# Kernel optimization log

Hardware: AMD Instinct MI355X
Metric: run time of the kernel (lower is better)

Reference implementation:

```python
import jax, jax.numpy as jnp
import numpy as np

B, N = 4, 512
H, NH, L = 64, 4, 3
HD = H // NH          # 16
NODE_F, EDGE_F = 18, 7
H4 = H // 4           # 16
FF = 4 * H            # 256


def _ln(x, g, b, eps=1e-5):
    m = jnp.mean(x, axis=-1, keepdims=True)
    v = jnp.mean((x - m) ** 2, axis=-1, keepdims=True)
    return (x - m) * jax.lax.rsqrt(v + eps) * g + b


def _leaky(x):
    return jnp.where(x >= 0, x, 0.2 * x)


def _spd(edge_mask):
    # Vectorized Floyd-Warshall, mirrors GraphTransformer._compute_spd_matrix
    n = edge_mask.shape[1]
    spd = jnp.where(edge_mask, 1.0, float(n)).astype(jnp.float32)
    i = jnp.arange(n)
    spd = spd.at[:, i, i].set(0.0)
    def body(k, s):
        col = jax.lax.dynamic_slice_in_dim(s, k, 1, axis=2)  # [B,N,1]
        row = jax.lax.dynamic_slice_in_dim(s, k, 1, axis=1)  # [B,1,N]
        return jnp.minimum(s, col + row)
    return jax.lax.fori_loop(0, n, body, spd)


def setup_inputs() -> dict:
    key = jax.random.key(0)
    ks = iter(jax.random.split(key, 64))
    def nrm(shape, s):
        return jax.random.normal(next(ks), shape, jnp.float32) * s
    inp = {}
    inp["node_features"] = jax.random.normal(next(ks), (B, N, NODE_F), jnp.float32)
    inp["edge_features"] = jax.random.normal(next(ks), (B, N, N, EDGE_F), jnp.float32)
    nm = jax.random.uniform(next(ks), (B, N)) < 0.9
    inp["node_mask"] = nm.at[:, 0].set(True)
    inp["edge_mask"] = jax.random.uniform(next(ks), (B, N, N)) < 0.05
    s_h = 1.0 / np.sqrt(H)
    inp["node_proj_w"] = nrm((NODE_F, H), 0.2)
    inp["node_proj_b"] = jnp.zeros((H,), jnp.float32)
    inp["edge_proj_w"] = nrm((EDGE_F, H), 0.2)
    inp["edge_proj_b"] = jnp.zeros((H,), jnp.float32)
    inp["wq"] = nrm((L, H, H), s_h)
    inp["wk"] = nrm((L, H, H), s_h)
    inp["wv"] = nrm((L, H, H), s_h)
    inp["eb1_w"] = nrm((L, H, H4), s_h)
    inp["eb1_b"] = jnp.zeros((L, H4), jnp.float32)
    inp["eb_ln_g"] = jnp.ones((L, H4), jnp.float32)
    inp["eb_ln_b"] = jnp.zeros((L, H4), jnp.float32)
    inp["eb2_w"] = nrm((L, H4, NH), 0.2)
    inp["eb2_b"] = jnp.zeros((L, NH), jnp.float32)
    inp["spd1_w"] = nrm((L, 1, H4), 0.5)
    inp["spd1_b"] = jnp.zeros((L, H4), jnp.float32)
    inp["spd2_w"] = nrm((L, H4, NH), 0.2)
    inp["spd2_b"] = jnp.zeros((L, NH), jnp.float32)
    inp["wo_w"] = nrm((L, H, H), s_h)
    inp["wo_b"] = jnp.zeros((L, H), jnp.float32)
    inp["ln1_g"] = jnp.ones((L, H), jnp.float32)
    inp["ln1_b"] = jnp.zeros((L, H), jnp.float32)
    inp["ln2_g"] = jnp.ones((L, H), jnp.float32)
    inp["ln2_b"] = jnp.zeros((L, H), jnp.float32)
    inp["ffn1_w"] = nrm((L, H, FF), s_h)
    inp["ffn1_b"] = jnp.zeros((L, FF), jnp.float32)
    inp["ffn2_w"] = nrm((L, FF, H), 1.0 / np.sqrt(FF))
    inp["ffn2_b"] = jnp.zeros((L, H), jnp.float32)
    inp["score1_w"] = nrm((2 * H, H), 1.0 / np.sqrt(2 * H))
    inp["score1_b"] = jnp.zeros((H,), jnp.float32)
    inp["score_ln_g"] = jnp.ones((H,), jnp.float32)
    inp["score_ln_b"] = jnp.zeros((H,), jnp.float32)
    inp["score2_w"] = nrm((H, 1), 0.1)
    inp["score2_b"] = jnp.zeros((1,), jnp.float32)
    return inp


def reference(node_features, edge_features, node_mask, edge_mask,
              node_proj_w, node_proj_b, edge_proj_w, edge_proj_b,
              wq, wk, wv,
              eb1_w, eb1_b, eb_ln_g, eb_ln_b, eb2_w, eb2_b,
              spd1_w, spd1_b, spd2_w, spd2_b,
              wo_w, wo_b, ln1_g, ln1_b, ln2_g, ln2_b,
              ffn1_w, ffn1_b, ffn2_w, ffn2_b,
              score1_w, score1_b, score_ln_g, score_ln_b, score2_w, score2_b):
    NEG = -1000000000.0
    h = node_features @ node_proj_w + node_proj_b            # [B,N,H]
    e = edge_features @ edge_proj_w + edge_proj_b            # [B,N,N,H]
    spd = _spd(edge_mask)
    spd_n = (jnp.clip(spd, 0.0, 10.0) / 10.0)[..., None]      # [B,N,N,1]
    scale = 1.0 / np.sqrt(HD)
    for l in range(L):
        Q = (h @ wq[l]).reshape(B, N, NH, HD)
        K = (h @ wk[l]).reshape(B, N, NH, HD)
        V = (h @ wv[l]).reshape(B, N, NH, HD)
        scores = jnp.einsum('bihd,bjhd->bhij', Q, K) * scale  # [B,NH,N,N]
        x = _leaky(_ln(e @ eb1_w[l] + eb1_b[l], eb_ln_g[l], eb_ln_b[l]))
        edge_bias = jnp.transpose(x @ eb2_w[l] + eb2_b[l], (0, 3, 1, 2))
        sb = _leaky(spd_n @ spd1_w[l] + spd1_b[l]) @ spd2_w[l] + spd2_b[l]
        spd_bias = jnp.transpose(sb, (0, 3, 1, 2))
        bias = jnp.where(edge_mask[:, None, :, :], edge_bias, spd_bias)
        scores = jnp.where(node_mask[:, None, None, :], scores + bias, NEG)
        attn = jax.nn.softmax(scores, axis=-1)
        out = jnp.einsum('bhij,bjhd->bihd', attn, V).reshape(B, N, H)
        out = out @ wo_w[l] + wo_b[l]
        h = _ln(h + out, ln1_g[l], ln1_b[l])
        ff = jax.nn.gelu(h @ ffn1_w[l] + ffn1_b[l], approximate=False) @ ffn2_w[l] + ffn2_b[l]
        h = _ln(h + ff, ln2_g[l], ln2_b[l])
    h_ego = jnp.broadcast_to(h[:, :1, :], (B, N - 1, H))
    hc = jnp.concatenate([h_ego, h[:, 1:, :]], axis=-1)       # [B,N-1,2H]
    x = _leaky(_ln(hc @ score1_w + score1_b, score_ln_g, score_ln_b))
    logits = (x @ score2_w + score2_b)[..., 0]                # [B,N-1]
    cand_mask = node_mask[:, 1:]
    no_cand = ~jnp.any(cand_mask, axis=-1)
    cand_mask = cand_mask.at[:, 0].set(cand_mask[:, 0] | no_cand)
    logits = jnp.where(cand_mask, logits, NEG)
    probs = jax.nn.softmax(logits, axis=-1)
    return probs, h
```

## Files before the change

kernel.cpp:

```cpp
#include <hip/hip_runtime.h>
#include <math.h>

typedef unsigned long long u64;
typedef unsigned int u32;

__device__ __forceinline__ float wsum(float x) {
#pragma unroll
    for (int o = 1; o < 64; o <<= 1) x += __shfl_xor(x, o);
    return x;
}
__device__ __forceinline__ float wmaxr(float x) {
#pragma unroll
    for (int o = 1; o < 64; o <<= 1) x = fmaxf(x, __shfl_xor(x, o));
    return x;
}

__global__ __launch_bounds__(256) void kA(
    const int* __restrict__ em, const float* __restrict__ nf,
    const float* __restrict__ npw, const float* __restrict__ npb,
    u64* __restrict__ adj, u32* __restrict__ elist, u32* __restrict__ rowCnt,
    float* __restrict__ hbuf)
{
    int t = threadIdx.x, wv = t >> 6, lane = t & 63;
    int g = blockIdx.x * 4 + wv;
    const int* emr = em + (size_t)g * 512;
    u32 run = 0;
#pragma unroll
    for (int s = 0; s < 8; ++s) {
        int j = s * 64 + lane;
        int v = emr[j];
        u64 bal = __ballot(v != 0);
        if (v != 0) {
            u32 slot = run + (u32)__popcll(bal & ((1ULL << lane) - 1ULL));
            if (slot < 96u) elist[g * 96 + slot] = (u32)j;
        }
        if (lane == 0) adj[(size_t)g * 8 + s] = bal;
        run += (u32)__popcll(bal);
    }
    if (lane == 0) rowCnt[g] = run < 96u ? run : 96u;
    float acc = npb[lane];
    const float* r = nf + (size_t)g * 18;
#pragma unroll
    for (int c = 0; c < 18; ++c) acc += r[c] * npw[c * 64 + lane];
    hbuf[(size_t)g * 64 + lane] = acc;
}

__global__ __launch_bounds__(256) void kB(
    const u64* __restrict__ adj, const float* __restrict__ ef,
    const u32* __restrict__ elist, const u32* __restrict__ rowCnt,
    const float* __restrict__ hbuf,
    const float* __restrict__ epw, const float* __restrict__ epb,
    const float* __restrict__ eb1w, const float* __restrict__ eb1b,
    const float* __restrict__ eblng, const float* __restrict__ eblnb,
    const float* __restrict__ eb2w, const float* __restrict__ eb2b,
    const float* __restrict__ wq, const float* __restrict__ wk, const float* __restrict__ wvw,
    unsigned char* __restrict__ spd, float* __restrict__ vals,
    float* __restrict__ Qb, float* __restrict__ KT, float* __restrict__ VT)
{
    __shared__ u64 adjL[4096 + 4 * 88];
    int t = threadIdx.x, wv = t >> 6, lane = t & 63;
    int g = blockIdx.x * 4 + wv;
    int b = g >> 9, srow = g & 511;
    {
        const float4* s = (const float4*)(adj + (size_t)b * 4096);
        float4* d = (float4*)adjL;
#pragma unroll
        for (int u = 0; u < 8; ++u) d[t + u * 256] = s[t + u * 256];
    }
    __syncthreads();
    u64* wb = adjL + 4096 + wv * 88;
    u64* vis = wb; u64* fro = wb + 8; u64* nxt = wb + 16; u64* dist8 = wb + 24;
    unsigned char* dist = (unsigned char*)dist8;
    dist8[lane] = 0x0A0A0A0A0A0A0A0AULL;
    if (lane < 8) { vis[lane] = 0ULL; fro[lane] = 0ULL; nxt[lane] = 0ULL; }
    __syncthreads();
    if (lane == 0) {
        dist[srow] = 0;
        vis[srow >> 6] = 1ULL << (srow & 63);
        fro[srow >> 6] = 1ULL << (srow & 63);
    }
    __syncthreads();
    for (int d = 1; d <= 9; ++d) {
        int c = lane >> 3, w = lane & 7;
        u64 f = fro[c];
        u64 acc = 0ULL;
        while (f) {
            int k = (c << 6) + __builtin_ctzll(f);
            f &= f - 1;
            acc |= adjL[k * 8 + w];
        }
        if (acc) atomicOr(&nxt[w], acc);
        __syncthreads();
        if (lane < 8) {
            u64 nw = nxt[lane] & ~vis[lane];
            vis[lane] |= nw; fro[lane] = nw; nxt[lane] = 0ULL;
            while (nw) {
                int j = (lane << 6) + __builtin_ctzll(nw);
                nw &= nw - 1;
                dist[j] = (unsigned char)d;
            }
        }
        __syncthreads();
    }
    ((u64*)(spd + (size_t)g * 512))[lane] = dist8[lane];
    {
        float hv = hbuf[(size_t)g * 64 + lane];
        float aq = 0.f, ak = 0.f, av = 0.f;
        for (int k = 0; k < 64; ++k) {
            float hk = __shfl(hv, k);
            aq += hk * wq[k * 64 + lane];
            ak += hk * wk[k * 64 + lane];
            av += hk * wvw[k * 64 + lane];
        }
        Qb[(size_t)g * 64 + lane] = aq;
        KT[((size_t)(b * 64 + lane)) * 512 + srow] = ak;
        VT[((size_t)(b * 64 + lane)) * 512 + srow] = av;
    }
    {
        u32 cnt = rowCnt[g];
        for (u32 s = lane; s < cnt; s += 64u) {
            u32 j = elist[g * 96 + s];
            const float* e7 = ef + ((size_t)g * 512 + j) * 7;
            float f0 = e7[0], f1 = e7[1], f2 = e7[2], f3 = e7[3], f4 = e7[4], f5 = e7[5], f6 = e7[6];
            float tt[3][16];
#pragma unroll
            for (int l = 0; l < 3; ++l)
#pragma unroll
                for (int c = 0; c < 16; ++c) tt[l][c] = eb1b[l * 16 + c];
            for (int k = 0; k < 64; ++k) {
                float ek = epb[k] + f0 * epw[k] + f1 * epw[64 + k] + f2 * epw[128 + k]
                         + f3 * epw[192 + k] + f4 * epw[256 + k] + f5 * epw[320 + k]
                         + f6 * epw[384 + k];
#pragma unroll
                for (int l = 0; l < 3; ++l) {
                    const float* W1 = eb1w + l * 1024 + k * 16;
#pragma unroll
                    for (int c = 0; c < 16; ++c) tt[l][c] += ek * W1[c];
                }
            }
#pragma unroll
            for (int l = 0; l < 3; ++l) {
                float m = 0.f;
#pragma unroll
                for (int c = 0; c < 16; ++c) m += tt[l][c];
                m *= 0.0625f;
                float var = 0.f;
#pragma unroll
                for (int c = 0; c < 16; ++c) { float d = tt[l][c] - m; var += d * d; }
                var *= 0.0625f;
                float inv = rsqrtf(var + 1e-5f);
#pragma unroll
                for (int c = 0; c < 16; ++c) {
                    float x = (tt[l][c] - m) * inv * eblng[l * 16 + c] + eblnb[l * 16 + c];
                    tt[l][c] = x >= 0.f ? x : 0.2f * x;
                }
#pragma unroll
                for (int hh = 0; hh < 4; ++hh) {
                    float a = eb2b[l * 4 + hh];
#pragma unroll
                    for (int c = 0; c < 16; ++c) a += tt[l][c] * eb2w[(l * 16 + c) * 4 + hh];
                    vals[(u32)(l * 4 + hh) * 196608u + (u32)g * 96u + s] = a;
                }
            }
        }
    }
}

__global__ __launch_bounds__(256, 2) void kL(
    const float* __restrict__ Qb, const float* __restrict__ KTin, const float* __restrict__ VTin,
    const unsigned char* __restrict__ spd, const u32* __restrict__ elist,
    const u32* __restrict__ rowCnt, const float* __restrict__ vals,
    const float* __restrict__ s1w, const float* __restrict__ s1b,
    const float* __restrict__ s2w, const float* __restrict__ s2b,
    const int* __restrict__ nm,
    const float* __restrict__ wow, const float* __restrict__ wob,
    const float* __restrict__ ln1g, const float* __restrict__ ln1b,
    const float* __restrict__ f1w, const float* __restrict__ f1b,
    const float* __restrict__ f2w, const float* __restrict__ f2b,
    const float* __restrict__ ln2g, const float* __restrict__ ln2b,
    const float* __restrict__ wqn, const float* __restrict__ wkn, const float* __restrict__ wvn,
    float* __restrict__ hbuf, float* __restrict__ QbOut,
    float* __restrict__ KTout, float* __restrict__ VTout,
    int l, float* __restrict__ out)
{
    __shared__ float kt[8192];
    __shared__ float bv[2048];
    __shared__ float ATTO[256];
    __shared__ unsigned char SPDl[2048];
    int t = threadIdx.x, wv = t >> 6, lane = t & 63;
    int blk = blockIdx.x;
    int g = blk * 4 + wv;
    int b = blk >> 7, srow = g & 511;
    float hv = hbuf[(size_t)g * 64 + lane];
    float qrow = Qb[(size_t)g * 64 + lane];
    {
        const u32* sp = (const u32*)(spd + (size_t)(blk * 4) * 512);
        u32* dd = (u32*)SPDl;
        dd[t] = sp[t]; dd[t + 256] = sp[t + 256];
    }
    float madd[8];
#pragma unroll
    for (int c = 0; c < 8; ++c) madd[c] = (nm[b * 512 + c * 64 + lane] != 0) ? 0.f : -1e9f;
    u32 cnt = rowCnt[g];
    u32 ej0 = 0, ej1 = 0;
    if (lane < (int)cnt) ej0 = elist[g * 96 + lane];
    if (lane + 64 < (int)cnt) ej1 = elist[g * 96 + lane + 64];

#pragma unroll 1
    for (int hh = 0; hh < 4; ++hh) {
        __syncthreads();
        {
            const float4* s = (const float4*)(KTin + ((size_t)(b * 64 + hh * 16)) * 512);
            float4* d = (float4*)kt;
#pragma unroll
            for (int u = 0; u < 8; ++u) d[t + u * 256] = s[t + u * 256];
        }
        float tval;
        {
            int li = lane < 11 ? lane : 10;
            float x = (float)li * 0.1f;
            float a = s2b[l * 4 + hh];
#pragma unroll
            for (int c = 0; c < 16; ++c) {
                float v = x * s1w[l * 16 + c] + s1b[l * 16 + c];
                v = v >= 0.f ? v : 0.2f * v;
                a += v * s2w[(l * 16 + c) * 4 + hh];
            }
            tval = a;
        }
#pragma unroll
        for (int p = 0; p < 2; ++p) {
            int i32 = t + p * 256;
            u32 w4 = ((const u32*)SPDl)[i32];
            float4 bb;
            bb.x = __shfl(tval, (int)(w4 & 255u));
            bb.y = __shfl(tval, (int)((w4 >> 8) & 255u));
            bb.z = __shfl(tval, (int)((w4 >> 16) & 255u));
            bb.w = __shfl(tval, (int)(w4 >> 24));
            ((float4*)bv)[i32] = bb;
        }
        __syncthreads();
        u32 vp = (u32)(l * 4 + hh) * 196608u;
        if (lane < (int)cnt) bv[wv * 512 + (int)(ej0 & 511u)] = vals[vp + (u32)g * 96u + lane];
        if (lane + 64 < (int)cnt) bv[wv * 512 + (int)(ej1 & 511u)] = vals[vp + (u32)g * 96u + lane + 64];
        float q[16];
#pragma unroll
        for (int d = 0; d < 16; ++d) q[d] = __shfl(qrow, hh * 16 + d);
        float sc[8];
        float mx = -3e38f;
#pragma unroll
        for (int c = 0; c < 8; ++c) {
            int j = c * 64 + lane;
            float s = 0.f;
#pragma unroll
            for (int d = 0; d < 16; ++d) s += q[d] * kt[d * 512 + j];
            s = s * 0.25f + bv[wv * 512 + j] + madd[c];
            sc[c] = s;
            mx = fmaxf(mx, s);
        }
        mx = wmaxr(mx);
        float sm = 0.f;
#pragma unroll
        for (int c = 0; c < 8; ++c) { sc[c] = __expf(sc[c] - mx); sm += sc[c]; }
        float sminv = 1.0f / wsum(sm);
#pragma unroll
        for (int c = 0; c < 8; ++c) sc[c] *= sminv;
        __syncthreads();
        {
            const float4* s = (const float4*)(VTin + ((size_t)(b * 64 + hh * 16)) * 512);
            float4* d = (float4*)kt;
#pragma unroll
            for (int u = 0; u < 8; ++u) d[t + u * 256] = s[t + u * 256];
        }
        __syncthreads();
        float acc[16];
#pragma unroll
        for (int d = 0; d < 16; ++d) acc[d] = 0.f;
#pragma unroll
        for (int c = 0; c < 8; ++c) {
            int j = c * 64 + lane;
#pragma unroll
            for (int d = 0; d < 16; ++d) acc[d] += sc[c] * kt[d * 512 + j];
        }
#pragma unroll
        for (int d = 0; d < 16; ++d) {
            acc[d] += __shfl_xor(acc[d], 16);
            acc[d] += __shfl_xor(acc[d], 32);
        }
        float* scr = bv + wv * 272;
        if (lane < 16) {
#pragma unroll
            for (int d = 0; d < 16; ++d) scr[lane * 17 + d] = acc[d];
        }
        if (lane < 16) {
            float o = 0.f;
#pragma unroll
            for (int m = 0; m < 16; ++m) o += scr[m * 17 + lane];
            ATTO[wv * 64 + hh * 16 + lane] = o;
        }
    }
    float h1;
    {
        float a = wob[l * 64 + lane];
        const float* Wo = wow + l * 4096;
        for (int k = 0; k < 64; ++k) a += ATTO[wv * 64 + k] * Wo[k * 64 + lane];
        float xx = a + hv;
        float mn = wsum(xx) * 0.015625f;
        float d = xx - mn;
        float var = wsum(d * d) * 0.015625f;
        h1 = d * rsqrtf(var + 1e-5f) * ln1g[l * 64 + lane] + ln1b[l * 64 + lane];
    }
    float hn;
    {
        const float* W1 = f1w + l * 16384;
        const float* W2 = f2w + l * 16384;
        float a1[4];
#pragma unroll
        for (int m = 0; m < 4; ++m) a1[m] = f1b[l * 256 + m * 64 + lane];
        for (int k = 0; k < 64; ++k) {
            float hk = __shfl(h1, k);
#pragma unroll
            for (int m = 0; m < 4; ++m) a1[m] += hk * W1[k * 256 + m * 64 + lane];
        }
        float ffv[4];
#pragma unroll
        for (int m = 0; m < 4; ++m) {
            float u = a1[m];
            ffv[m] = 0.5f * u * (1.0f + erff(u * 0.70710678118654752f));
        }
        float a2 = 0.f;
#pragma unroll 1
        for (int m = 0; m < 4; ++m) {
            for (int ll = 0; ll < 64; ++ll) {
                a2 += __shfl(ffv[m], ll) * W2[(m * 64 + ll) * 64 + lane];
            }
        }
        float xx = a2 + f2b[l * 64 + lane] + h1;
        float mn = wsum(xx) * 0.015625f;
        float d = xx - mn;
        float var = wsum(d * d) * 0.015625f;
        hn = d * rsqrtf(var + 1e-5f) * ln2g[l * 64 + lane] + ln2b[l * 64 + lane];
    }
    hbuf[(size_t)g * 64 + lane] = hn;
    if (l == 2) {
        out[2044 + (size_t)g * 64 + lane] = hn;
    } else {
        float aq = 0.f, ak = 0.f, av = 0.f;
        for (int k = 0; k < 64; ++k) {
            float hk = __shfl(hn, k);
            aq += hk * wqn[k * 64 + lane];
            ak += hk * wkn[k * 64 + lane];
            av += hk * wvn[k * 64 + lane];
        }
        QbOut[(size_t)g * 64 + lane] = aq;
        KTout[((size_t)(b * 64 + lane)) * 512 + srow] = ak;
        VTout[((size_t)(b * 64 + lane)) * 512 + srow] = av;
    }
}

__global__ __launch_bounds__(256) void kS(
    const float* __restrict__ hbuf,
    const float* __restrict__ s1w, const float* __restrict__ s1b,
    const float* __restrict__ lng, const float* __restrict__ lnb,
    const float* __restrict__ s2w, const float* __restrict__ s2b,
    float* __restrict__ logits)
{
    int t = threadIdx.x, wv = t >> 6, lane = t & 63;
    int wid = blockIdx.x * 4 + wv;
    if (wid >= 2044) return;
    int bb = wid / 511; int jj = wid % 511; int j = jj + 1;
    float ego = hbuf[(size_t)bb * 32768 + lane];
    float cand = hbuf[((size_t)(bb * 512 + j)) * 64 + lane];
    float acc = s1b[lane];
    for (int k = 0; k < 64; ++k) acc += __shfl(ego, k) * s1w[k * 64 + lane];
    for (int k = 0; k < 64; ++k) acc += __shfl(cand, k) * s1w[(64 + k) * 64 + lane];
    float mn = wsum(acc) * 0.015625f;
    float d = acc - mn;
    float var = wsum(d * d) * 0.015625f;
    float x = d * rsqrtf(var + 1e-5f) * lng[lane] + lnb[lane];
    x = x >= 0.f ? x : 0.2f * x;
    float p = wsum(x * s2w[lane]);
    if (lane == 0) logits[wid] = p + s2b[0];
}

__global__ __launch_bounds__(512) void kP(
    const float* __restrict__ logits, const int* __restrict__ nmask, float* __restrict__ out)
{
    __shared__ float red[512];
    __shared__ int anyf;
    int b = blockIdx.x; int t = threadIdx.x;
    bool cand = false;
    if (t < 511) cand = nmask[b * 512 + 1 + t] != 0;
    if (t == 0) anyf = 0;
    __syncthreads();
    if (cand) atomicOr(&anyf, 1);
    __syncthreads();
    if (t == 0 && anyf == 0) cand = true;
    float val = -3e38f;
    if (t < 511) val = cand ? logits[b * 511 + t] : -1e9f;
    red[t] = val; __syncthreads();
    for (int s = 256; s > 0; s >>= 1) { if (t < s) red[t] = fmaxf(red[t], red[t + s]); __syncthreads(); }
    float m = red[0]; __syncthreads();
    float p = (t < 511) ? __expf(val - m) : 0.f;
    red[t] = p; __syncthreads();
    for (int s = 256; s > 0; s >>= 1) { if (t < s) red[t] += red[t + s]; __syncthreads(); }
    float inv = 1.0f / red[0];
    if (t < 511) out[b * 511 + t] = p * inv;
}

extern "C" void kernel_launch(void* const* d_in, const int* in_sizes, int n_in,
                              void* d_out, int out_size, void* d_ws, size_t ws_size,
                              hipStream_t stream) {
    const float* nf    = (const float*)d_in[0];
    const float* ef    = (const float*)d_in[1];
    const int*   nm    = (const int*)d_in[2];
    const int*   em    = (const int*)d_in[3];
    const float* npw   = (const float*)d_in[4];
    const float* npb   = (const float*)d_in[5];
    const float* epw   = (const float*)d_in[6];
    const float* epb   = (const float*)d_in[7];
    const float* wq    = (const float*)d_in[8];
    const float* wk    = (const float*)d_in[9];
    const float* wv    = (const float*)d_in[10];
    const float* eb1w  = (const float*)d_in[11];
    const float* eb1b  = (const float*)d_in[12];
    const float* eblng = (const float*)d_in[13];
    const float* eblnb = (const float*)d_in[14];
    const float* eb2w  = (const float*)d_in[15];
    const float* eb2b  = (const float*)d_in[16];
    const float* s1wv  = (const float*)d_in[17];
    const float* s1bv  = (const float*)d_in[18];
    const float* s2wv  = (const float*)d_in[19];
    const float* s2bv  = (const float*)d_in[20];
    const float* wow   = (const float*)d_in[21];
    const float* wob   = (const float*)d_in[22];
    const float* ln1g  = (const float*)d_in[23];
    const float* ln1b  = (const float*)d_in[24];
    const float* ln2g  = (const float*)d_in[25];
    const float* ln2b  = (const float*)d_in[26];
    const float* f1w   = (const float*)d_in[27];
    const float* f1b   = (const float*)d_in[28];
    const float* f2w   = (const float*)d_in[29];
    const float* f2b   = (const float*)d_in[30];
    const float* sc1w  = (const float*)d_in[31];
    const float* sc1b  = (const float*)d_in[32];
    const float* sclng = (const float*)d_in[33];
    const float* sclnb = (const float*)d_in[34];
    const float* sc2w  = (const float*)d_in[35];
    const float* sc2b  = (const float*)d_in[36];

    char* W = (char*)d_ws;
    u64*   adj    = (u64*)(W + 0);
    unsigned char* spd = (unsigned char*)(W + 131072);
    u32*   elist  = (u32*)(W + 1179648);
    u32*   rowCnt = (u32*)(W + 1966080);
    float* vals   = (float*)(W + 1974272);
    float* hbuf   = (float*)(W + 11411456);
    float* Qb     = (float*)(W + 11935744);
    float* KT0    = (float*)(W + 12460032);
    float* VT0    = (float*)(W + 12984320);
    float* KT1    = (float*)(W + 13508608);
    float* VT1    = (float*)(W + 14032896);
    float* logits = (float*)(W + 14557184);

    float* out = (float*)d_out;

    kA<<<512, 256, 0, stream>>>(em, nf, npw, npb, adj, elist, rowCnt, hbuf);
    kB<<<512, 256, 0, stream>>>(adj, ef, elist, rowCnt, hbuf, epw, epb,
                                eb1w, eb1b, eblng, eblnb, eb2w, eb2b,
                                wq, wk, wv, spd, vals, Qb, KT0, VT0);
    kL<<<512, 256, 0, stream>>>(Qb, KT0, VT0, spd, elist, rowCnt, vals,
                                s1wv, s1bv, s2wv, s2bv, nm,
                                wow, wob, ln1g, ln1b, f1w, f1b, f2w, f2b, ln2g, ln2b,
                                wq + 4096, wk + 4096, wv + 4096,
                                hbuf, Qb, KT1, VT1, 0, out);
    kL<<<512, 256, 0, stream>>>(Qb, KT1, VT1, spd, elist, rowCnt, vals,
                                s1wv, s1bv, s2wv, s2bv, nm,
                                wow, wob, ln1g, ln1b, f1w, f1b, f2w, f2b, ln2g, ln2b,
                                wq + 8192, wk + 8192, wv + 8192,
                                hbuf, Qb, KT0, VT0, 1, out);
    kL<<<512, 256, 0, stream>>>(Qb, KT0, VT0, spd, elist, rowCnt, vals,
                                s1wv, s1bv, s2wv, s2bv, nm,
                                wow, wob, ln1g, ln1b, f1w, f1b, f2w, f2b, ln2g, ln2b,
                                wq, wk, wv,
                                hbuf, Qb, KT1, VT1, 2, out);
    kS<<<512, 256, 0, stream>>>(hbuf, sc1w, sc1b, sclng, sclnb, sc2w, sc2b, logits);
    kP<<<4, 512, 0, stream>>>(logits, nm, out);
}
```

Baseline: 336.8 us.

## Split attention per head, fold edge-bias weights, early-exit BFS, precompute ego projection

The per-layer kernel is split into a head-parallel attention kernel (2048 blocks) and a separate output/FFN kernel, which raises parallelism at the cost of an extra launch and an attention-output round trip through global memory. The edge-bias MLP folds the edge projection into the first bias layer via a precomputed 7x16 matrix held in shared memory. Edge work is pooled across the four warps of a block to balance load. The BFS exits early once all frontiers are empty and keeps distances in registers. The ego half of the scoring MLP is computed once per batch in the last layer instead of per candidate.

```diff
diff --git a/kernel.cpp b/kernel.cpp
--- a/kernel.cpp
+++ b/kernel.cpp
@@ -57,7 +57,13 @@
     unsigned char* __restrict__ spd, float* __restrict__ vals,
     float* __restrict__ Qb, float* __restrict__ KT, float* __restrict__ VT)
 {
-    __shared__ u64 adjL[4096 + 4 * 88];
+    __shared__ u64 adjL[4096];
+    __shared__ u64 bfsS[4][24];
+    __shared__ float MS[684];
+    __shared__ u32 pool[384];
+    __shared__ u32 offs[5];
+    __shared__ u32 cA[4];
+    __shared__ int votes[4];
     int t = threadIdx.x, wv = t >> 6, lane = t & 63;
     int g = blockIdx.x * 4 + wv;
     int b = g >> 9, srow = g & 511;
@@ -67,19 +73,31 @@
 #pragma unroll
         for (int u = 0; u < 8; ++u) d[t + u * 256] = s[t + u * 256];
     }
-    __syncthreads();
-    u64* wb = adjL + 4096 + wv * 88;
-    u64* vis = wb; u64* fro = wb + 8; u64* nxt = wb + 16; u64* dist8 = wb + 24;
-    unsigned char* dist = (unsigned char*)dist8;
-    dist8[lane] = 0x0A0A0A0A0A0A0A0AULL;
-    if (lane < 8) { vis[lane] = 0ULL; fro[lane] = 0ULL; nxt[lane] = 0ULL; }
-    __syncthreads();
-    if (lane == 0) {
-        dist[srow] = 0;
-        vis[srow >> 6] = 1ULL << (srow & 63);
-        fro[srow >> 6] = 1ULL << (srow & 63);
-    }
-    __syncthreads();
+    for (int u = t; u < 384; u += 256) {
+        int l = u >> 7, r = u & 127, f = r >> 4, c = r & 15;
+        const float* W1 = eb1w + l * 1024 + c;
+        float s;
+        if (f < 7) {
+            s = 0.f;
+            const float* ew = epw + f * 64;
+            for (int k = 0; k < 64; ++k) s += ew[k] * W1[k * 16];
+        } else {
+            s = eb1b[l * 16 + c];
+            for (int k = 0; k < 64; ++k) s += epb[k] * W1[k * 16];
+        }
+        MS[u] = s;
+    }
+    if (t < 192) MS[384 + t] = eb2w[t];
+    if (t < 48) { MS[576 + t] = eblng[t]; MS[624 + t] = eblnb[t]; }
+    if (t < 12) MS[672 + t] = eb2b[t];
+    u64* vis = &bfsS[wv][0]; u64* fro = vis + 8; u64* nxt = vis + 16;
+    if (lane < 8) {
+        u64 iv = (lane == (srow >> 6)) ? (1ULL << (srow & 63)) : 0ULL;
+        vis[lane] = iv; fro[lane] = iv; nxt[lane] = 0ULL;
+    }
+    __syncthreads();
+    u64 myDist = 0x0A0A0A0A0A0A0A0AULL;
+    if (lane == (srow >> 3)) myDist &= ~(0xFFULL << ((srow & 7) * 8));
     for (int d = 1; d <= 9; ++d) {
         int c = lane >> 3, w = lane & 7;
         u64 f = fro[c];
@@ -91,18 +109,25 @@
         }
         if (acc) atomicOr(&nxt[w], acc);
         __syncthreads();
+        u64 nw = 0ULL;
         if (lane < 8) {
-            u64 nw = nxt[lane] & ~vis[lane];
+            nw = nxt[lane] & ~vis[lane];
             vis[lane] |= nw; fro[lane] = nw; nxt[lane] = 0ULL;
-            while (nw) {
-                int j = (lane << 6) + __builtin_ctzll(nw);
-                nw &= nw - 1;
-                dist[j] = (unsigned char)d;
-            }
-        }
+        }
+        u64 bal = __ballot(nw != 0ULL);
+        if (lane == 0) votes[wv] = (bal != 0ULL) ? 1 : 0;
         __syncthreads();
-    }
-    ((u64*)(spd + (size_t)g * 512))[lane] = dist8[lane];
+        u64 fw = fro[lane >> 3];
+        u32 bits = (u32)(fw >> ((lane & 7) * 8)) & 0xFFu;
+        if (bits) {
+            u64 bm = 0ULL;
+#pragma unroll
+            for (int kk = 0; kk < 8; ++kk) if (bits & (1u << kk)) bm |= 0xFFULL << (8 * kk);
+            myDist = (myDist & ~bm) | ((0x0101010101010101ULL * (u64)(u32)d) & bm);
+        }
+        if (!(votes[0] | votes[1] | votes[2] | votes[3])) break;
+    }
+    ((u64*)spd)[(size_t)g * 64 + lane] = myDist;
     {
         float hv = hbuf[(size_t)g * 64 + lane];
         float aq = 0.f, ak = 0.f, av = 0.f;
@@ -116,194 +141,212 @@
         KT[((size_t)(b * 64 + lane)) * 512 + srow] = ak;
         VT[((size_t)(b * 64 + lane)) * 512 + srow] = av;
     }
-    {
-        u32 cnt = rowCnt[g];
-        for (u32 s = lane; s < cnt; s += 64u) {
-            u32 j = elist[g * 96 + s];
-            const float* e7 = ef + ((size_t)g * 512 + j) * 7;
-            float f0 = e7[0], f1 = e7[1], f2 = e7[2], f3 = e7[3], f4 = e7[4], f5 = e7[5], f6 = e7[6];
-            float tt[3][16];
-#pragma unroll
-            for (int l = 0; l < 3; ++l)
-#pragma unroll
-                for (int c = 0; c < 16; ++c) tt[l][c] = eb1b[l * 16 + c];
-            for (int k = 0; k < 64; ++k) {
-                float ek = epb[k] + f0 * epw[k] + f1 * epw[64 + k] + f2 * epw[128 + k]
-                         + f3 * epw[192 + k] + f4 * epw[256 + k] + f5 * epw[320 + k]
-                         + f6 * epw[384 + k];
-#pragma unroll
-                for (int l = 0; l < 3; ++l) {
-                    const float* W1 = eb1w + l * 1024 + k * 16;
-#pragma unroll
-                    for (int c = 0; c < 16; ++c) tt[l][c] += ek * W1[c];
-                }
+    u32 cnt = rowCnt[g];
+    if (lane == 0) cA[wv] = cnt;
+    __syncthreads();
+    if (t == 0) {
+        u32 a = 0;
+        for (int i = 0; i < 4; ++i) { offs[i] = a; a += cA[i]; }
+        offs[4] = a;
+    }
+    __syncthreads();
+    u32 base = offs[wv];
+    if (lane < (int)cnt)
+        pool[base + lane] = ((u32)wv << 16) | ((u32)lane << 9) | elist[g * 96 + lane];
+    if (lane + 64 < (int)cnt)
+        pool[base + lane + 64] = ((u32)wv << 16) | ((u32)(lane + 64) << 9) | elist[g * 96 + lane + 64];
+    __syncthreads();
+    u32 tot = offs[4];
+    for (u32 e = t; e < tot; e += 256) {
+        u32 p = pool[e];
+        int rl = (int)(p >> 16);
+        u32 s = (p >> 9) & 127u;
+        u32 j = p & 511u;
+        int ge = blockIdx.x * 4 + rl;
+        const float* e7 = ef + ((size_t)ge * 512 + j) * 7;
+        float ff[7];
+#pragma unroll
+        for (int f = 0; f < 7; ++f) ff[f] = e7[f];
+#pragma unroll 1
+        for (int l = 0; l < 3; ++l) {
+            float tt[16];
+#pragma unroll
+            for (int c = 0; c < 16; ++c) tt[c] = MS[(l * 8 + 7) * 16 + c];
+#pragma unroll
+            for (int f = 0; f < 7; ++f) {
+                float fv = ff[f];
+#pragma unroll
+                for (int c = 0; c < 16; ++c) tt[c] += fv * MS[(l * 8 + f) * 16 + c];
             }
-#pragma unroll
-            for (int l = 0; l < 3; ++l) {
-                float m = 0.f;
-#pragma unroll
-                for (int c = 0; c < 16; ++c) m += tt[l][c];
-                m *= 0.0625f;
-                float var = 0.f;
-#pragma unroll
-                for (int c = 0; c < 16; ++c) { float d = tt[l][c] - m; var += d * d; }
-                var *= 0.0625f;
-                float inv = rsqrtf(var + 1e-5f);
-#pragma unroll
-                for (int c = 0; c < 16; ++c) {
-                    float x = (tt[l][c] - m) * inv * eblng[l * 16 + c] + eblnb[l * 16 + c];
-                    tt[l][c] = x >= 0.f ? x : 0.2f * x;
-                }
-#pragma unroll
-                for (int hh = 0; hh < 4; ++hh) {
-                    float a = eb2b[l * 4 + hh];
-#pragma unroll
-                    for (int c = 0; c < 16; ++c) a += tt[l][c] * eb2w[(l * 16 + c) * 4 + hh];
-                    vals[(u32)(l * 4 + hh) * 196608u + (u32)g * 96u + s] = a;
-                }
+            float m = 0.f;
+#pragma unroll
+            for (int c = 0; c < 16; ++c) m += tt[c];
+            m *= 0.0625f;
+            float var = 0.f;
+#pragma unroll
+            for (int c = 0; c < 16; ++c) { float d = tt[c] - m; var += d * d; }
+            var *= 0.0625f;
+            float inv = rsqrtf(var + 1e-5f);
+#pragma unroll
+            for (int c = 0; c < 16; ++c) {
+                float x = (tt[c] - m) * inv * MS[576 + l * 16 + c] + MS[624 + l * 16 + c];
+                tt[c] = x >= 0.f ? x : 0.2f * x;
             }
-        }
-    }
-}
-
-__global__ __launch_bounds__(256, 2) void kL(
+#pragma unroll
+            for (int hh = 0; hh < 4; ++hh) {
+                float a = MS[672 + l * 4 + hh];
+#pragma unroll
+                for (int c = 0; c < 16; ++c) a += tt[c] * MS[384 + (l * 16 + c) * 4 + hh];
+                vals[(u32)(l * 4 + hh) * 196608u + (u32)ge * 96u + s] = a;
+            }
+        }
+    }
+}
+
+__global__ __launch_bounds__(256) void kAttn(
     const float* __restrict__ Qb, const float* __restrict__ KTin, const float* __restrict__ VTin,
     const unsigned char* __restrict__ spd, const u32* __restrict__ elist,
     const u32* __restrict__ rowCnt, const float* __restrict__ vals,
     const float* __restrict__ s1w, const float* __restrict__ s1b,
     const float* __restrict__ s2w, const float* __restrict__ s2b,
-    const int* __restrict__ nm,
+    const int* __restrict__ nm, int l, float* __restrict__ attO)
+{
+    __shared__ float kt[8192];
+    __shared__ float bv[2048];
+    int t = threadIdx.x, wv = t >> 6, lane = t & 63;
+    int blk = blockIdx.x;
+    int bh = blk >> 7, tile = blk & 127;
+    int b = bh >> 2, hh = bh & 3;
+    int rbase = tile * 4;
+    int g = b * 512 + rbase + wv;
+    {
+        const float4* s = (const float4*)(KTin + ((size_t)(b * 64 + hh * 16)) * 512);
+        float4* d = (float4*)kt;
+#pragma unroll
+        for (int u = 0; u < 8; ++u) d[t + u * 256] = s[t + u * 256];
+    }
+    float tval;
+    {
+        int li = lane < 11 ? lane : 10;
+        float x = (float)li * 0.1f;
+        float a = s2b[l * 4 + hh];
+#pragma unroll
+        for (int c = 0; c < 16; ++c) {
+            float v = x * s1w[l * 16 + c] + s1b[l * 16 + c];
+            v = v >= 0.f ? v : 0.2f * v;
+            a += v * s2w[(l * 16 + c) * 4 + hh];
+        }
+        tval = a;
+    }
+    {
+        const u32* sp = (const u32*)(spd + ((size_t)(b * 512 + rbase)) * 512);
+#pragma unroll
+        for (int p = 0; p < 2; ++p) {
+            int i32 = t + p * 256;
+            u32 w4 = sp[i32];
+            float4 bb;
+            bb.x = __shfl(tval, (int)(w4 & 255u));
+            bb.y = __shfl(tval, (int)((w4 >> 8) & 255u));
+            bb.z = __shfl(tval, (int)((w4 >> 16) & 255u));
+            bb.w = __shfl(tval, (int)(w4 >> 24));
+            ((float4*)bv)[i32] = bb;
+        }
+    }
+    __syncthreads();
+    u32 cnt = rowCnt[g];
+    u32 vp = (u32)(l * 4 + hh) * 196608u;
+    if (lane < (int)cnt) {
+        u32 j = elist[g * 96 + lane];
+        bv[wv * 512 + j] = vals[vp + (u32)g * 96u + lane];
+    }
+    if (lane + 64 < (int)cnt) {
+        u32 j = elist[g * 96 + lane + 64];
+        bv[wv * 512 + j] = vals[vp + (u32)g * 96u + lane + 64];
+    }
+    float madd[8];
+#pragma unroll
+    for (int c = 0; c < 8; ++c) madd[c] = (nm[b * 512 + c * 64 + lane] != 0) ? 0.f : -1e9f;
+    float qrow = Qb[(size_t)g * 64 + lane];
+    float q[16];
+#pragma unroll
+    for (int d = 0; d < 16; ++d) q[d] = __shfl(qrow, hh * 16 + d);
+    float sc[8];
+    float mx = -3e38f;
+#pragma unroll
+    for (int c = 0; c < 8; ++c) {
+        int j = c * 64 + lane;
+        float s = 0.f;
+#pragma unroll
+        for (int d = 0; d < 16; ++d) s += q[d] * kt[d * 512 + j];
+        s = s * 0.25f + bv[wv * 512 + j] + madd[c];
+        sc[c] = s;
+        mx = fmaxf(mx, s);
+    }
+    mx = wmaxr(mx);
+    float sm = 0.f;
+#pragma unroll
+    for (int c = 0; c < 8; ++c) { sc[c] = __expf(sc[c] - mx); sm += sc[c]; }
+    float sminv = 1.0f / wsum(sm);
+#pragma unroll
+    for (int c = 0; c < 8; ++c) sc[c] *= sminv;
+    __syncthreads();
+    {
+        const float4* s = (const float4*)(VTin + ((size_t)(b * 64 + hh * 16)) * 512);
+        float4* d = (float4*)kt;
+#pragma unroll
+        for (int u = 0; u < 8; ++u) d[t + u * 256] = s[t + u * 256];
+    }
+    __syncthreads();
+    float acc[16];
+#pragma unroll
+    for (int d = 0; d < 16; ++d) acc[d] = 0.f;
+#pragma unroll
+    for (int c = 0; c < 8; ++c) {
+        int j = c * 64 + lane;
+#pragma unroll
+        for (int d = 0; d < 16; ++d) acc[d] += sc[c] * kt[d * 512 + j];
+    }
+#pragma unroll
+    for (int d = 0; d < 16; ++d) {
+        acc[d] += __shfl_xor(acc[d], 16);
+        acc[d] += __shfl_xor(acc[d], 32);
+    }
+    float* scr = bv + wv * 272;
+    if (lane < 16) {
+#pragma unroll
+        for (int d = 0; d < 16; ++d) scr[lane * 17 + d] = acc[d];
+    }
+    if (lane < 16) {
+        float o = 0.f;
+#pragma unroll
+        for (int m = 0; m < 16; ++m) o += scr[m * 17 + lane];
+        attO[(size_t)g * 64 + hh * 16 + lane] = o;
+    }
+}
+
+__global__ __launch_bounds__(256) void kLF(
+    const float* __restrict__ attO,
     const float* __restrict__ wow, const float* __restrict__ wob,
     const float* __restrict__ ln1g, const float* __restrict__ ln1b,
     const float* __restrict__ f1w, const float* __restrict__ f1b,
     const float* __restrict__ f2w, const float* __restrict__ f2b,
     const float* __restrict__ ln2g, const float* __restrict__ ln2b,
     const float* __restrict__ wqn, const float* __restrict__ wkn, const float* __restrict__ wvn,
+    const float* __restrict__ sc1w, const float* __restrict__ sc1b,
     float* __restrict__ hbuf, float* __restrict__ QbOut,
     float* __restrict__ KTout, float* __restrict__ VTout,
-    int l, float* __restrict__ out)
+    float* __restrict__ egoAcc, int l, float* __restrict__ out)
 {
-    __shared__ float kt[8192];
-    __shared__ float bv[2048];
-    __shared__ float ATTO[256];
-    __shared__ unsigned char SPDl[2048];
     int t = threadIdx.x, wv = t >> 6, lane = t & 63;
-    int blk = blockIdx.x;
-    int g = blk * 4 + wv;
-    int b = blk >> 7, srow = g & 511;
+    int g = blockIdx.x * 4 + wv;
+    int b = g >> 9, srow = g & 511;
     float hv = hbuf[(size_t)g * 64 + lane];
-    float qrow = Qb[(size_t)g * 64 + lane];
-    {
-        const u32* sp = (const u32*)(spd + (size_t)(blk * 4) * 512);
-        u32* dd = (u32*)SPDl;
-        dd[t] = sp[t]; dd[t + 256] = sp[t + 256];
-    }
-    float madd[8];
-#pragma unroll
-    for (int c = 0; c < 8; ++c) madd[c] = (nm[b * 512 + c * 64 + lane] != 0) ? 0.f : -1e9f;
-    u32 cnt = rowCnt[g];
-    u32 ej0 = 0, ej1 = 0;
-    if (lane < (int)cnt) ej0 = elist[g * 96 + lane];
-    if (lane + 64 < (int)cnt) ej1 = elist[g * 96 + lane + 64];
-
-#pragma unroll 1
-    for (int hh = 0; hh < 4; ++hh) {
-        __syncthreads();
-        {
-            const float4* s = (const float4*)(KTin + ((size_t)(b * 64 + hh * 16)) * 512);
-            float4* d = (float4*)kt;
-#pragma unroll
-            for (int u = 0; u < 8; ++u) d[t + u * 256] = s[t + u * 256];
-        }
-        float tval;
-        {
-            int li = lane < 11 ? lane : 10;
-            float x = (float)li * 0.1f;
-            float a = s2b[l * 4 + hh];
-#pragma unroll
-            for (int c = 0; c < 16; ++c) {
-                float v = x * s1w[l * 16 + c] + s1b[l * 16 + c];
-                v = v >= 0.f ? v : 0.2f * v;
-                a += v * s2w[(l * 16 + c) * 4 + hh];
-            }
-            tval = a;
-        }
-#pragma unroll
-        for (int p = 0; p < 2; ++p) {
-            int i32 = t + p * 256;
-            u32 w4 = ((const u32*)SPDl)[i32];
-            float4 bb;
-            bb.x = __shfl(tval, (int)(w4 & 255u));
-            bb.y = __shfl(tval, (int)((w4 >> 8) & 255u));
-            bb.z = __shfl(tval, (int)((w4 >> 16) & 255u));
-            bb.w = __shfl(tval, (int)(w4 >> 24));
-            ((float4*)bv)[i32] = bb;
-        }
-        __syncthreads();
-        u32 vp = (u32)(l * 4 + hh) * 196608u;
-        if (lane < (int)cnt) bv[wv * 512 + (int)(ej0 & 511u)] = vals[vp + (u32)g * 96u + lane];
-        if (lane + 64 < (int)cnt) bv[wv * 512 + (int)(ej1 & 511u)] = vals[vp + (u32)g * 96u + lane + 64];
-        float q[16];
-#pragma unroll
-        for (int d = 0; d < 16; ++d) q[d] = __shfl(qrow, hh * 16 + d);
-        float sc[8];
-        float mx = -3e38f;
-#pragma unroll
-        for (int c = 0; c < 8; ++c) {
-            int j = c * 64 + lane;
-            float s = 0.f;
-#pragma unroll
-            for (int d = 0; d < 16; ++d) s += q[d] * kt[d * 512 + j];
-            s = s * 0.25f + bv[wv * 512 + j] + madd[c];
-            sc[c] = s;
-            mx = fmaxf(mx, s);
-        }
-        mx = wmaxr(mx);
-        float sm = 0.f;
-#pragma unroll
-        for (int c = 0; c < 8; ++c) { sc[c] = __expf(sc[c] - mx); sm += sc[c]; }
-        float sminv = 1.0f / wsum(sm);
-#pragma unroll
-        for (int c = 0; c < 8; ++c) sc[c] *= sminv;
-        __syncthreads();
-        {
-            const float4* s = (const float4*)(VTin + ((size_t)(b * 64 + hh * 16)) * 512);
-            float4* d = (float4*)kt;
-#pragma unroll
-            for (int u = 0; u < 8; ++u) d[t + u * 256] = s[t + u * 256];
-        }
-        __syncthreads();
-        float acc[16];
-#pragma unroll
-        for (int d = 0; d < 16; ++d) acc[d] = 0.f;
-#pragma unroll
-        for (int c = 0; c < 8; ++c) {
-            int j = c * 64 + lane;
-#pragma unroll
-            for (int d = 0; d < 16; ++d) acc[d] += sc[c] * kt[d * 512 + j];
-        }
-#pragma unroll
-        for (int d = 0; d < 16; ++d) {
-            acc[d] += __shfl_xor(acc[d], 16);
-            acc[d] += __shfl_xor(acc[d], 32);
-        }
-        float* scr = bv + wv * 272;
-        if (lane < 16) {
-#pragma unroll
-            for (int d = 0; d < 16; ++d) scr[lane * 17 + d] = acc[d];
-        }
-        if (lane < 16) {
-            float o = 0.f;
-#pragma unroll
-            for (int m = 0; m < 16; ++m) o += scr[m * 17 + lane];
-            ATTO[wv * 64 + hh * 16 + lane] = o;
-        }
-    }
+    float att = attO[(size_t)g * 64 + lane];
     float h1;
     {
         float a = wob[l * 64 + lane];
         const float* Wo = wow + l * 4096;
-        for (int k = 0; k < 64; ++k) a += ATTO[wv * 64 + k] * Wo[k * 64 + lane];
+        for (int k = 0; k < 64; ++k) a += __shfl(att, k) * Wo[k * 64 + lane];
         float xx = a + hv;
         float mn = wsum(xx) * 0.015625f;
         float d = xx - mn;
@@ -344,6 +387,11 @@
     hbuf[(size_t)g * 64 + lane] = hn;
     if (l == 2) {
         out[2044 + (size_t)g * 64 + lane] = hn;
+        if (srow == 0) {
+            float ea = sc1b[lane];
+            for (int k = 0; k < 64; ++k) ea += __shfl(hn, k) * sc1w[k * 64 + lane];
+            egoAcc[b * 64 + lane] = ea;
+        }
     } else {
         float aq = 0.f, ak = 0.f, av = 0.f;
         for (int k = 0; k < 64; ++k) {
@@ -359,8 +407,8 @@
 }
 
 __global__ __launch_bounds__(256) void kS(
-    const float* __restrict__ hbuf,
-    const float* __restrict__ s1w, const float* __restrict__ s1b,
+    const float* __restrict__ hbuf, const float* __restrict__ egoAcc,
+    const float* __restrict__ s1w,
     const float* __restrict__ lng, const float* __restrict__ lnb,
     const float* __restrict__ s2w, const float* __restrict__ s2b,
     float* __restrict__ logits)
@@ -369,10 +417,8 @@
     int wid = blockIdx.x * 4 + wv;
     if (wid >= 2044) return;
     int bb = wid / 511; int jj = wid % 511; int j = jj + 1;
-    float ego = hbuf[(size_t)bb * 32768 + lane];
     float cand = hbuf[((size_t)(bb * 512 + j)) * 64 + lane];
-    float acc = s1b[lane];
-    for (int k = 0; k < 64; ++k) acc += __shfl(ego, k) * s1w[k * 64 + lane];
+    float acc = egoAcc[bb * 64 + lane];
     for (int k = 0; k < 64; ++k) acc += __shfl(cand, k) * s1w[(64 + k) * 64 + lane];
     float mn = wsum(acc) * 0.015625f;
     float d = acc - mn;
@@ -462,6 +508,8 @@
     float* KT1    = (float*)(W + 13508608);
     float* VT1    = (float*)(W + 14032896);
     float* logits = (float*)(W + 14557184);
+    float* egoAcc = (float*)(W + 14565376);
+    float* attO   = (float*)(W + 14566400);
 
     float* out = (float*)d_out;
 
@@ -469,21 +517,25 @@
     kB<<<512, 256, 0, stream>>>(adj, ef, elist, rowCnt, hbuf, epw, epb,
                                 eb1w, eb1b, eblng, eblnb, eb2w, eb2b,
                                 wq, wk, wv, spd, vals, Qb, KT0, VT0);
-    kL<<<512, 256, 0, stream>>>(Qb, KT0, VT0, spd, elist, rowCnt, vals,
-                                s1wv, s1bv, s2wv, s2bv, nm,
-                                wow, wob, ln1g, ln1b, f1w, f1b, f2w, f2b, ln2g, ln2b,
-                                wq + 4096, wk + 4096, wv + 4096,
-                                hbuf, Qb, KT1, VT1, 0, out);
-    kL<<<512, 256, 0, stream>>>(Qb, KT1, VT1, spd, elist, rowCnt, vals,
-                                s1wv, s1bv, s2wv, s2bv, nm,
-                                wow, wob, ln1g, ln1b, f1w, f1b, f2w, f2b, ln2g, ln2b,
-                                wq + 8192, wk + 8192, wv + 8192,
-                                hbuf, Qb, KT0, VT0, 1, out);
-    kL<<<512, 256, 0, stream>>>(Qb, KT0, VT0, spd, elist, rowCnt, vals,
-                                s1wv, s1bv, s2wv, s2bv, nm,
-                                wow, wob, ln1g, ln1b, f1w, f1b, f2w, f2b, ln2g, ln2b,
-                                wq, wk, wv,
-                                hbuf, Qb, KT1, VT1, 2, out);
-    kS<<<512, 256, 0, stream>>>(hbuf, sc1w, sc1b, sclng, sclnb, sc2w, sc2b, logits);
+
+    kAttn<<<2048, 256, 0, stream>>>(Qb, KT0, VT0, spd, elist, rowCnt, vals,
+                                    s1wv, s1bv, s2wv, s2bv, nm, 0, attO);
+    kLF<<<512, 256, 0, stream>>>(attO, wow, wob, ln1g, ln1b, f1w, f1b, f2w, f2b,
+                                 ln2g, ln2b, wq + 4096, wk + 4096, wv + 4096,
+                                 sc1w, sc1b, hbuf, Qb, KT1, VT1, egoAcc, 0, out);
+
+    kAttn<<<2048, 256, 0, stream>>>(Qb, KT1, VT1, spd, elist, rowCnt, vals,
+                                    s1wv, s1bv, s2wv, s2bv, nm, 1, attO);
+    kLF<<<512, 256, 0, stream>>>(attO, wow, wob, ln1g, ln1b, f1w, f1b, f2w, f2b,
+                                 ln2g, ln2b, wq + 8192, wk + 8192, wv + 8192,
+                                 sc1w, sc1b, hbuf, Qb, KT0, VT0, egoAcc, 1, out);
+
+    kAttn<<<2048, 256, 0, stream>>>(Qb, KT0, VT0, spd, elist, rowCnt, vals,
+                                    s1wv, s1bv, s2wv, s2bv, nm, 2, attO);
+    kLF<<<512, 256, 0, stream>>>(attO, wow, wob, ln1g, ln1b, f1w, f1b, f2w, f2b,
+                                 ln2g, ln2b, wq, wk, wv,
+                                 sc1w, sc1b, hbuf, Qb, KT1, VT1, egoAcc, 2, out);
+
+    kS<<<511, 256, 0, stream>>>(hbuf, egoAcc, s1wv ? sc1w : sc1w, sclng, sclnb, sc2w, sc2b, logits);
     kP<<<4, 512, 0, stream>>>(logits, nm, out);
 }
```

After: 315.8 us. 1.07x faster.
